# Kernel optimization log

Measured on AMD Instinct MI355X. Metric: run time of the kernel, lower is better.

The kernel has to match this reference:

```python
import jax, jax.numpy as jnp
import numpy as np

NUM_CLASSES = 172
IGNORE_INDEX = 255
DICE_WEIGHT = 0.5
EPS = 1e-7


def setup_inputs() -> dict:
    key = jax.random.key(0)
    k1, k2 = jax.random.split(key)
    pred = jax.random.normal(k1, (4, NUM_CLASSES, 256, 256), dtype=jnp.float32)
    target = jax.random.randint(k2, (4, 256, 256), 0, NUM_CLASSES, dtype=jnp.int32)
    return {"pred": pred, "target": target}


def reference(pred, target):
    # pred: [B, C, H, W] logits; target: [B, H, W] int labels (255 = ignore)
    C = NUM_CLASSES
    logp = jax.nn.log_softmax(pred, axis=1)  # [B, C, H, W]

    # ---- cross entropy with ignore_index (mean over valid pixels) ----
    valid = target != IGNORE_INDEX  # [B, H, W]
    safe_tgt = jnp.where(valid, target, 0)
    nll = -jnp.take_along_axis(logp, safe_tgt[:, None].astype(jnp.int32), axis=1)[:, 0]  # [B, H, W]
    n_valid = jnp.sum(valid)
    ce = jnp.sum(jnp.where(valid, nll, 0.0)) / jnp.maximum(n_valid, 1).astype(pred.dtype)

    # ---- dice loss: vectorized over classes (replaces per-class python loop) ----
    p = jnp.exp(logp)  # softmax probs [B, C, H, W]
    # intersection[c] = sum over pixels with target==c of p[:, c] at those pixels
    gathered = jnp.take_along_axis(p, safe_tgt[:, None].astype(jnp.int32), axis=1)[:, 0]  # [B, H, W]
    seg_ids = target.ravel().astype(jnp.int32)  # ignore pixels land in bucket 255, discarded
    inter = jax.ops.segment_sum(gathered.ravel(), seg_ids, num_segments=256)[:C]  # [C]
    counts = jax.ops.segment_sum(jnp.ones_like(gathered.ravel()), seg_ids, num_segments=256)[:C]
    union = jnp.sum(p, axis=(0, 2, 3)) + counts  # [C]
    valid_c = union > 0
    dice_terms = jnp.where(valid_c, (2.0 * inter + EPS) / (union + EPS), 0.0)
    n_valid_c = jnp.sum(valid_c).astype(pred.dtype)
    dice = jnp.where(n_valid_c > 0, 1.0 - jnp.sum(dice_terms) / jnp.maximum(n_valid_c, 1.0), 0.0)

    return ce + DICE_WEIGHT * dice
```

## Files before the change

kernel.cpp:

```cpp
#include <hip/hip_runtime.h>
#include <stdint.h>

#define NCLS 172
#define IGN 255
#define HW 65536
#define NPIX 262144
#define EPSV 1e-7f
#define TP 32
#define TROWS 192
#define TSZ (TROWS * TP)
#define NTILE 4
#define PIXPERBLK (TP * NTILE)
#define NSTAGE 32
#define SS 520

__device__ __forceinline__ void gl_lds16(const float* g, float* l) {
    __builtin_amdgcn_global_load_lds(
        (const __attribute__((address_space(1))) void*)g,
        (__attribute__((address_space(3))) void*)l, 16, 0, 0);
}

__global__ __launch_bounds__(256) void seg_fused(
    const float* __restrict__ pred, const int* __restrict__ tgt,
    float* __restrict__ part)
{
    __shared__ float tile[2 * TSZ];
    __shared__ float sPart[128];
    __shared__ float sInvs[TP];
    __shared__ int   sTgt[PIXPERBLK];
    __shared__ float sInter[NCLS];
    __shared__ unsigned int sCnt[NCLS];

    const int tid   = threadIdx.x;
    const int lane  = tid & 63;
    const int wv    = tid >> 6;
    const int p     = tid & 31;
    const int chunk = tid >> 5;

    for (int i = tid; i < NCLS; i += 256) { sInter[i] = 0.f; sCnt[i] = 0u; }
    const int pix0 = blockIdx.x * PIXPERBLK;
    if (tid < PIXPERBLK) sTgt[tid] = tgt[pix0 + tid];

    const int b   = pix0 >> 16;
    const int hw0 = pix0 & (HW - 1);
    const float* gb = pred + (size_t)b * NCLS * HW + hw0;

    const int scb = lane >> 3;
    const int spo = (lane & 7) << 2;

    #pragma unroll
    for (int k = 0; k < 6; ++k) {
        const int ib = wv + 4 * k;
        int cb = ib * 8 + scb; if (cb > NCLS - 1) cb = NCLS - 1;
        gl_lds16(gb + (size_t)cb * HW + spo, &tile[ib * (8 * TP)]);
    }

    float unionAcc = 0.f, ceAcc = 0.f, nvAcc = 0.f;

    for (int tI = 0; tI < NTILE; ++tI) {
        const int tb = (tI & 1) * TSZ;

        if (tI + 1 < NTILE) {
            const float* gt = gb + (tI + 1) * TP;
            const int nb = ((tI + 1) & 1) * TSZ;
            #pragma unroll
            for (int k = 0; k < 6; ++k) {
                const int ib = wv + 4 * k;
                int cb = ib * 8 + scb; if (cb > NCLS - 1) cb = NCLS - 1;
                gl_lds16(gt + (size_t)cb * HW + spo, &tile[nb + ib * (8 * TP)]);
            }
            asm volatile("s_waitcnt vmcnt(6) lgkmcnt(0)" ::: "memory");
        } else {
            asm volatile("s_waitcnt vmcnt(0) lgkmcnt(0)" ::: "memory");
        }
        __builtin_amdgcn_s_barrier();
        __builtin_amdgcn_sched_barrier(0);

        float s0 = 0.f, s1 = 0.f;
        #pragma unroll
        for (int k = 0; k < 20; k += 2) {
            const int i0 = tb + (chunk + 8 * k) * TP + p;
            const int i1 = tb + (chunk + 8 * k + 8) * TP + p;
            const float e0 = __expf(tile[i0]);
            const float e1 = __expf(tile[i1]);
            tile[i0] = e0; tile[i1] = e1;
            s0 += e0; s1 += e1;
        }
        {   const int i0 = tb + (chunk + 160) * TP + p;
            const float e = __expf(tile[i0]); tile[i0] = e; s0 += e; }
        if (chunk < 4) {
            const int i1 = tb + (chunk + 168) * TP + p;
            const float e = __expf(tile[i1]); tile[i1] = e; s1 += e;
        }
        float sv = s0 + s1;
        sv += __shfl_down(sv, 32, 64);
        if (lane < 32) sPart[wv * 32 + p] = sv;
        asm volatile("s_waitcnt lgkmcnt(0)" ::: "memory");
        __builtin_amdgcn_s_barrier();
        __builtin_amdgcn_sched_barrier(0);

        if (tid < 32) {
            const float s    = (sPart[p] + sPart[32 + p]) + (sPart[64 + p] + sPart[96 + p]);
            const float invs = 1.0f / s;
            sInvs[p] = invs;
            const int  t     = sTgt[tI * TP + p];
            const bool valid = (t != IGN);
            const int  st    = valid ? t : 0;
            const float et   = tile[tb + st * TP + p];
            const float pt   = et * invs;
            float nll = valid ? -__logf(pt) : 0.f;
            float nv  = valid ? 1.f : 0.f;
            if (valid) { atomicAdd(&sInter[st], pt); atomicAdd(&sCnt[st], 1u); }
            #pragma unroll
            for (int off = 16; off > 0; off >>= 1) {
                nll += __shfl_down(nll, off, 64);
                nv  += __shfl_down(nv,  off, 64);
            }
            if (tid == 0) { ceAcc += nll; nvAcc += nv; }
        }
        asm volatile("s_waitcnt lgkmcnt(0)" ::: "memory");
        __builtin_amdgcn_s_barrier();
        __builtin_amdgcn_sched_barrier(0);

        if (tid < NCLS) {
            const int tr = tb + tid * TP;
            float u0 = 0.f, u1 = 0.f;
            #pragma unroll
            for (int k = 0; k < TP; k += 2) {
                const int p0 = (tid + k)     & (TP - 1);
                const int p1 = (tid + k + 1) & (TP - 1);
                u0 += tile[tr + p0] * sInvs[p0];
                u1 += tile[tr + p1] * sInvs[p1];
            }
            unionAcc += u0 + u1;
        }
        asm volatile("s_waitcnt lgkmcnt(0)" ::: "memory");
        __builtin_amdgcn_s_barrier();
        __builtin_amdgcn_sched_barrier(0);
    }

    float* pb = part + (size_t)(blockIdx.x & (NSTAGE - 1)) * SS;
    for (int i = tid; i < NCLS; i += 256) {
        const float vi = sInter[i];
        if (vi != 0.f) atomicAdd(&pb[i], vi);
        const unsigned int ci = sCnt[i];
        if (ci != 0u) atomicAdd(&pb[NCLS + i], (float)ci);
    }
    if (tid < NCLS) atomicAdd(&pb[344 + tid], unionAcc);
    if (tid == 0) { atomicAdd(&pb[516], ceAcc); atomicAdd(&pb[517], nvAcc); }
}

__global__ __launch_bounds__(256) void seg_fin(
    const float* __restrict__ part, float* __restrict__ out)
{
    __shared__ float sT[256], sN[256];
    const int tid = threadIdx.x;
    float term = 0.f, nv = 0.f;
    if (tid < NCLS) {
        float inter = 0.f, cnt = 0.f, uni = 0.f;
        for (int st = 0; st < NSTAGE; ++st) {
            inter += part[st * SS + tid];
            cnt   += part[st * SS + NCLS + tid];
            uni   += part[st * SS + 344 + tid];
        }
        const float u = uni + cnt;
        if (u > 0.f) { term = (2.f * inter + EPSV) / (u + EPSV); nv = 1.f; }
    }
    sT[tid] = term; sN[tid] = nv;
    __syncthreads();
    #pragma unroll
    for (int s2 = 128; s2 > 0; s2 >>= 1) {
        if (tid < s2) { sT[tid] += sT[tid + s2]; sN[tid] += sN[tid + s2]; }
        __syncthreads();
    }
    if (tid == 0) {
        float ce = 0.f, nvl = 0.f;
        for (int st = 0; st < NSTAGE; ++st) {
            ce  += part[st * SS + 516];
            nvl += part[st * SS + 517];
        }
        const float ceo  = ce / fmaxf(nvl, 1.f);
        const float dice = (sN[0] > 0.f) ? (1.f - sT[0] / fmaxf(sN[0], 1.f)) : 0.f;
        out[0] = ceo + 0.5f * dice;
    }
}

extern "C" void kernel_launch(void* const* d_in, const int* in_sizes, int n_in,
                              void* d_out, int out_size, void* d_ws, size_t ws_size,
                              hipStream_t stream) {
    const float* pred = (const float*)d_in[0];
    const int*   tgt  = (const int*)d_in[1];
    float* out  = (float*)d_out;
    float* part = (float*)d_ws;

    hipMemsetAsync(d_ws, 0, NSTAGE * SS * sizeof(float), stream);
    seg_fused<<<NPIX / PIXPERBLK, 256, 0, stream>>>(pred, tgt, part);
    seg_fin<<<1, 256, 0, stream>>>(part, out);
}
```

Baseline: 256.9 us.

## Keep softmax exponentials in registers and accumulate per-class union per thread

```diff
diff --git a/kernel.cpp b/kernel.cpp
--- a/kernel.cpp
+++ b/kernel.cpp
@@ -29,6 +29,7 @@
     __shared__ float sInvs[TP];
     __shared__ int   sTgt[PIXPERBLK];
     __shared__ float sInter[NCLS];
+    __shared__ float sUnion[NCLS];
     __shared__ unsigned int sCnt[NCLS];
 
     const int tid   = threadIdx.x;
@@ -36,10 +37,12 @@
     const int wv    = tid >> 6;
     const int p     = tid & 31;
     const int chunk = tid >> 5;
+    const bool has22 = (chunk < 4);
 
     for (int i = tid; i < NCLS; i += 256) { sInter[i] = 0.f; sCnt[i] = 0u; }
     const int pix0 = blockIdx.x * PIXPERBLK;
     if (tid < PIXPERBLK) sTgt[tid] = tgt[pix0 + tid];
+    asm volatile("" ::: "memory");
 
     const int b   = pix0 >> 16;
     const int hw0 = pix0 & (HW - 1);
@@ -55,7 +58,10 @@
         gl_lds16(gb + (size_t)cb * HW + spo, &tile[ib * (8 * TP)]);
     }
 
-    float unionAcc = 0.f, ceAcc = 0.f, nvAcc = 0.f;
+    float uAcc[22];
+    #pragma unroll
+    for (int k = 0; k < 22; ++k) uAcc[k] = 0.f;
+    float ceAcc = 0.f, nvAcc = 0.f;
 
     for (int tI = 0; tI < NTILE; ++tI) {
         const int tb = (tI & 1) * TSZ;
@@ -76,22 +82,17 @@
         __builtin_amdgcn_s_barrier();
         __builtin_amdgcn_sched_barrier(0);
 
+        float e[22];
         float s0 = 0.f, s1 = 0.f;
         #pragma unroll
         for (int k = 0; k < 20; k += 2) {
-            const int i0 = tb + (chunk + 8 * k) * TP + p;
-            const int i1 = tb + (chunk + 8 * k + 8) * TP + p;
-            const float e0 = __expf(tile[i0]);
-            const float e1 = __expf(tile[i1]);
-            tile[i0] = e0; tile[i1] = e1;
-            s0 += e0; s1 += e1;
-        }
-        {   const int i0 = tb + (chunk + 160) * TP + p;
-            const float e = __expf(tile[i0]); tile[i0] = e; s0 += e; }
-        if (chunk < 4) {
-            const int i1 = tb + (chunk + 168) * TP + p;
-            const float e = __expf(tile[i1]); tile[i1] = e; s1 += e;
-        }
+            e[k]     = __expf(tile[tb + (chunk + 8 * k)       * TP + p]);
+            e[k + 1] = __expf(tile[tb + (chunk + 8 * (k + 1)) * TP + p]);
+            s0 += e[k]; s1 += e[k + 1];
+        }
+        e[20] = __expf(tile[tb + (chunk + 160) * TP + p]); s0 += e[20];
+        if (has22) { e[21] = __expf(tile[tb + (chunk + 168) * TP + p]); s1 += e[21]; }
+        else       { e[21] = 0.f; }
         float sv = s0 + s1;
         sv += __shfl_down(sv, 32, 64);
         if (lane < 32) sPart[wv * 32 + p] = sv;
@@ -106,11 +107,10 @@
             const int  t     = sTgt[tI * TP + p];
             const bool valid = (t != IGN);
             const int  st    = valid ? t : 0;
-            const float et   = tile[tb + st * TP + p];
-            const float pt   = et * invs;
-            float nll = valid ? -__logf(pt) : 0.f;
+            const float xt   = tile[tb + st * TP + p];
+            float nll = valid ? (__logf(s) - xt) : 0.f;
             float nv  = valid ? 1.f : 0.f;
-            if (valid) { atomicAdd(&sInter[st], pt); atomicAdd(&sCnt[st], 1u); }
+            if (valid) { atomicAdd(&sInter[st], __expf(xt) * invs); atomicAdd(&sCnt[st], 1u); }
             #pragma unroll
             for (int off = 16; off > 0; off >>= 1) {
                 nll += __shfl_down(nll, off, 64);
@@ -122,22 +122,27 @@
         __builtin_amdgcn_s_barrier();
         __builtin_amdgcn_sched_barrier(0);
 
-        if (tid < NCLS) {
-            const int tr = tb + tid * TP;
-            float u0 = 0.f, u1 = 0.f;
-            #pragma unroll
-            for (int k = 0; k < TP; k += 2) {
-                const int p0 = (tid + k)     & (TP - 1);
-                const int p1 = (tid + k + 1) & (TP - 1);
-                u0 += tile[tr + p0] * sInvs[p0];
-                u1 += tile[tr + p1] * sInvs[p1];
-            }
-            unionAcc += u0 + u1;
-        }
-        asm volatile("s_waitcnt lgkmcnt(0)" ::: "memory");
-        __builtin_amdgcn_s_barrier();
-        __builtin_amdgcn_sched_barrier(0);
-    }
+        const float invs = sInvs[p];
+        #pragma unroll
+        for (int k = 0; k < 22; ++k) uAcc[k] += e[k] * invs;
+    }
+
+    #pragma unroll
+    for (int k = 0; k < 22; ++k) {
+        float v = uAcc[k];
+        #pragma unroll
+        for (int m = 16; m > 0; m >>= 1) v += __shfl_xor(v, m, 64);
+        uAcc[k] = v;
+    }
+    if (p == 0) {
+        #pragma unroll
+        for (int k = 0; k < 22; ++k) {
+            const int c = chunk + 8 * k;
+            if (c < NCLS) sUnion[c] = uAcc[k];
+        }
+    }
+    asm volatile("s_waitcnt lgkmcnt(0)" ::: "memory");
+    __builtin_amdgcn_s_barrier();
 
     float* pb = part + (size_t)(blockIdx.x & (NSTAGE - 1)) * SS;
     for (int i = tid; i < NCLS; i += 256) {
@@ -145,8 +150,8 @@
         if (vi != 0.f) atomicAdd(&pb[i], vi);
         const unsigned int ci = sCnt[i];
         if (ci != 0u) atomicAdd(&pb[NCLS + i], (float)ci);
-    }
-    if (tid < NCLS) atomicAdd(&pb[344 + tid], unionAcc);
+        atomicAdd(&pb[344 + i], sUnion[i]);
+    }
     if (tid == 0) { atomicAdd(&pb[516], ceAcc); atomicAdd(&pb[517], nvAcc); }
 }
 
```

New measurement: 257.3 us. No clear change (+0.1%).
